# Kernel optimization log

Hardware: AMD Instinct MI355X
Metric: run time of the kernel (lower is better)

Reference implementation:

```python
import jax, jax.numpy as jnp
import numpy as np
import math

A, B, C, D = 32, 32, 8, 16
K, STRIDE, PAD, ITERS = 3, 1, 1, 3
KK = K * K
KKA = KK * A


def squash(s, axis=-1):
    mag_sq = jnp.sum(s ** 2, axis=axis, keepdims=True)
    mag = jnp.sqrt(mag_sq)
    return mag_sq / (1.0 + mag_sq) * (s / mag)


def setup_inputs() -> dict:
    key = jax.random.key(0)
    k1, k2 = jax.random.split(key)
    pose = jax.random.normal(k1, (4, A * C, 14, 14), dtype=jnp.float32)
    # kaiming_uniform_ on (KKA, B*D, C): fan_in = (B*D)*C = 4096, bound = sqrt(6/fan_in)
    bound = math.sqrt(6.0 / (B * D * C))
    W = jax.random.uniform(k2, (KKA, B * D, C), dtype=jnp.float32, minval=-bound, maxval=bound)
    return {"pose": pose, "W": W}


def reference(pose, W):
    b, _, h, w = pose.shape
    # F.unfold equivalent: (b, A*C*kk, oh, ow), channel-major then kernel-position ordering
    patches = jax.lax.conv_general_dilated_patches(
        pose, (K, K), (STRIDE, STRIDE), [(PAD, PAD), (PAD, PAD)])
    l = patches.shape[2] * patches.shape[3]
    x = patches.reshape(b, A, C, KK, l)
    x = jnp.transpose(x, (0, 4, 3, 1, 2)).reshape(b, l, KKA, C)  # (b,l,kkA,C)
    # pose_out[b,l,k,:] = W[k] @ x[b,l,k]  -> (b,l,kkA,B*D)
    pose_out = jnp.einsum('kpc,blkc->blkp', W, x).reshape(b, l, KKA, B, D)
    logits = jnp.zeros((b, l, KKA, B, 1), dtype=pose.dtype)
    v = None
    for _ in range(ITERS):
        c = jax.nn.softmax(logits, axis=3)                      # over B capsules
        s = jnp.sum(c * pose_out, axis=2, keepdims=True)        # (b,l,1,B,D)
        v = squash(s)
        logits = logits + jnp.sum(v * pose_out, axis=-1, keepdims=True)
    v = v[:, :, 0]                                              # (b,l,B,D)
    v = jnp.transpose(v.reshape(b, l, B * D), (0, 2, 1))        # (b,B*D,l)
    oh = math.isqrt(l)
    return v.reshape(b, B * D, oh, oh)
```

## Files before the change

### kernel.cpp

```cpp
#include <hip/hip_runtime.h>
#include <stdint.h>

#define NSITES 784
#define LSZ    196
#define HWD    14
#define KKA_   288
#define BD_    512
#define NRG    6
#define ROWS_PER_BLK 48
#define NW     8
#define ROWS_PER_WAVE 6
#define SITES_PER_BLK 4

#define WH_OFF    0
#define XH_OFF    2359296
#define PART_OFF  5971968
#define VBUF_OFF  15605760
#define WS_NEED   17211392

typedef _Float16 h2 __attribute__((ext_vector_type(2)));

#define PIN8(p) asm volatile("" : "+v"(p[0]),"+v"(p[1]),"+v"(p[2]),"+v"(p[3]), \
                                  "+v"(p[4]),"+v"(p[5]),"+v"(p[6]),"+v"(p[7]))

__device__ __forceinline__ float dot8(const uint4 wv, const uint4 xv) {
    h2 w0 = __builtin_bit_cast(h2, wv.x), w1 = __builtin_bit_cast(h2, wv.y),
       w2 = __builtin_bit_cast(h2, wv.z), w3 = __builtin_bit_cast(h2, wv.w);
    h2 x0 = __builtin_bit_cast(h2, xv.x), x1 = __builtin_bit_cast(h2, xv.y),
       x2 = __builtin_bit_cast(h2, xv.z), x3 = __builtin_bit_cast(h2, xv.w);
#if __has_builtin(__builtin_amdgcn_fdot2)
    float acc = __builtin_amdgcn_fdot2(w0, x0, 0.f, false);
    acc = __builtin_amdgcn_fdot2(w1, x1, acc, false);
    acc = __builtin_amdgcn_fdot2(w2, x2, acc, false);
    acc = __builtin_amdgcn_fdot2(w3, x3, acc, false);
    return acc;
#else
    float acc = (float)w0.x*(float)x0.x + (float)w0.y*(float)x0.y
              + (float)w1.x*(float)x1.x + (float)w1.y*(float)x1.y
              + (float)w2.x*(float)x2.x + (float)w2.y*(float)x2.y
              + (float)w3.x*(float)x3.x + (float)w3.y*(float)x3.y;
    return acc;
#endif
}

__global__ __launch_bounds__(256) void k_prep(
    const float* __restrict__ pose, const float* __restrict__ W,
    uint4* __restrict__ Wh, uint4* __restrict__ xh)
{
    const int t  = threadIdx.x;
    const int bx = blockIdx.x;
    if (bx < NSITES) {
        const int site = bx;
        const int b = site / LSZ;
        const int l = site - b * LSZ;
        const int oh = l / HWD, ow = l - oh * HWD;
        for (int kk = t; kk < KKA_; kk += 256) {
            const int p = kk >> 5, a = kk & 31;
            const int ky = p / 3 - 1, kx = p % 3 - 1;
            const int y = oh + ky, x = ow + kx;
            const bool inb = (y >= 0 && y < HWD && x >= 0 && x < HWD);
            const float* pp = pose + ((size_t)b * 256 + a * 8) * LSZ
                            + (inb ? (y * HWD + x) : 0);
            uint32_t uo[4];
            #pragma unroll
            for (int cp = 0; cp < 4; ++cp) {
                const float f0 = inb ? pp[(2*cp)   * LSZ] : 0.f;
                const float f1 = inb ? pp[(2*cp+1) * LSZ] : 0.f;
                h2 hh; hh.x = (_Float16)f0; hh.y = (_Float16)f1;
                uo[cp] = __builtin_bit_cast(uint32_t, hh);
            }
            uint4 o; o.x = uo[0]; o.y = uo[1]; o.z = uo[2]; o.w = uo[3];
            xh[(size_t)site * KKA_ + kk] = o;
        }
    } else {
        const int wb = bx - NSITES;
        const int kk = wb * 4 + (t >> 6);
        const int ln = t & 63;
        const float* Wr = W + (size_t)kk * (BD_ * 8);
        #pragma unroll
        for (int u = 0; u < 8; ++u) {
            const int p = ln * 8 + u;
            const float4 fa = *(const float4*)(Wr + p * 8);
            const float4 fb = *(const float4*)(Wr + p * 8 + 4);
            uint32_t uo[4];
            h2 h0; h0.x=(_Float16)fa.x; h0.y=(_Float16)fa.y; uo[0]=__builtin_bit_cast(uint32_t,h0);
            h2 h1; h1.x=(_Float16)fa.z; h1.y=(_Float16)fa.w; uo[1]=__builtin_bit_cast(uint32_t,h1);
            h2 hv; hv.x=(_Float16)fb.x; hv.y=(_Float16)fb.y; uo[2]=__builtin_bit_cast(uint32_t,hv);
            h2 h3; h3.x=(_Float16)fb.z; h3.y=(_Float16)fb.w; uo[3]=__builtin_bit_cast(uint32_t,h3);
            uint4 o; o.x=uo[0]; o.y=uo[1]; o.z=uo[2]; o.w=uo[3];
            Wh[(size_t)kk * 512 + u * 64 + ln] = o;
        }
    }
}

template<int PASS>
__global__ __launch_bounds__(512, 4) void k_sweep(
    const uint4* __restrict__ Wh, const uint4* __restrict__ xh,
    const float* __restrict__ vbuf, float* __restrict__ partial)
{
    const int t  = threadIdx.x;
    const int w  = t >> 6;
    const int ln = t & 63;
    const int sg = blockIdx.x;
    const int rg = blockIdx.y;
    const int site0 = sg * SITES_PER_BLK;
    const int kk0 = __builtin_amdgcn_readfirstlane(rg * ROWS_PER_BLK + w);

    float v[SITES_PER_BLK][8];
    if (PASS >= 2) {
        #pragma unroll
        for (int s = 0; s < SITES_PER_BLK; ++s) {
            const float4* vp = (const float4*)(vbuf + (size_t)(site0 + s) * BD_ + ln * 8);
            const float4 a = vp[0], bq = vp[1];
            v[s][0]=a.x;  v[s][1]=a.y;  v[s][2]=a.z;  v[s][3]=a.w;
            v[s][4]=bq.x; v[s][5]=bq.y; v[s][6]=bq.z; v[s][7]=bq.w;
            PIN8(v[s]);
        }
    }

    float sacc[SITES_PER_BLK][8];
    #pragma unroll
    for (int s = 0; s < SITES_PER_BLK; ++s)
        #pragma unroll
        for (int j = 0; j < 8; ++j) sacc[s][j] = 0.f;

    const uint4* Wrow = Wh + (size_t)kk0 * 512;
    const uint4* xrow = xh + kk0;

    #pragma unroll 1
    for (int r = 0; r < ROWS_PER_WAVE; ++r) {
        uint4 wr[8];
        #pragma unroll
        for (int u = 0; u < 8; ++u) wr[u] = Wrow[u * 64 + ln];
        Wrow += NW * 512;

        #pragma unroll
        for (int s = 0; s < SITES_PER_BLK; ++s) {
            const uint4 xr = xrow[(size_t)(site0 + s) * KKA_];
            float po[8];
            #pragma unroll
            for (int j = 0; j < 8; ++j) po[j] = dot8(wr[j], xr);
            if (PASS == 1) {
                #pragma unroll
                for (int j = 0; j < 8; ++j) sacc[s][j] += po[j];
            } else {
                float up = v[s][0] * po[0];
                #pragma unroll
                for (int j = 1; j < 8; ++j) up += v[s][j] * po[j];
                up += __shfl_xor(up, 1, 64);
                const float e = __expf(up);
                float se = e;
                se += __shfl_xor(se, 2, 64);
                se += __shfl_xor(se, 4, 64);
                se += __shfl_xor(se, 8, 64);
                se += __shfl_xor(se, 16, 64);
                se += __shfl_xor(se, 32, 64);
                const float c = e * __builtin_amdgcn_rcpf(se);
                #pragma unroll
                for (int j = 0; j < 8; ++j) sacc[s][j] += c * po[j];
            }
        }
        xrow += NW;
    }

    __shared__ float red[NW * BD_];
    #pragma unroll
    for (int s = 0; s < SITES_PER_BLK; ++s) {
        if (s) __syncthreads();
        float4 r0, r1;
        r0.x=sacc[s][0]; r0.y=sacc[s][1]; r0.z=sacc[s][2]; r0.w=sacc[s][3];
        r1.x=sacc[s][4]; r1.y=sacc[s][5]; r1.z=sacc[s][6]; r1.w=sacc[s][7];
        *(float4*)&red[w * BD_ + ln * 8]     = r0;
        *(float4*)&red[w * BD_ + ln * 8 + 4] = r1;
        __syncthreads();
        {
            const int p = t;
            float acc = red[p];
            #pragma unroll
            for (int ww = 1; ww < NW; ++ww) acc += red[ww * BD_ + p];
            partial[((size_t)(site0 + s) * NRG + rg) * BD_ + p] = acc;
        }
    }
}

template<int PASS>
__global__ __launch_bounds__(256) void k_reduce(
    const float* __restrict__ partial, float* __restrict__ vbuf,
    float* __restrict__ out)
{
    const int site = blockIdx.x * 4 + (threadIdx.x >> 6);
    const int ln = threadIdx.x & 63;
    float tv[8] = {0.f,0.f,0.f,0.f,0.f,0.f,0.f,0.f};
    #pragma unroll
    for (int rg = 0; rg < NRG; ++rg) {
        const float4* pp4 = (const float4*)(partial + ((size_t)site * NRG + rg) * BD_ + ln * 8);
        const float4 a = pp4[0], b = pp4[1];
        tv[0]+=a.x; tv[1]+=a.y; tv[2]+=a.z; tv[3]+=a.w;
        tv[4]+=b.x; tv[5]+=b.y; tv[6]+=b.z; tv[7]+=b.w;
    }
    if (PASS == 1) {
        #pragma unroll
        for (int j = 0; j < 8; ++j) tv[j] *= (1.f / 32.f);
    }
    float msq = 0.f;
    #pragma unroll
    for (int j = 0; j < 8; ++j) msq += tv[j] * tv[j];
    msq += __shfl_xor(msq, 1, 64);
    const float fac = sqrtf(msq) / (1.f + msq);
    if (PASS == 1) {
        #pragma unroll
        for (int j = 0; j < 8; ++j) vbuf[(size_t)site * BD_ + ln * 8 + j] = tv[j] * fac;
    } else if (PASS == 2) {
        #pragma unroll
        for (int j = 0; j < 8; ++j) vbuf[(size_t)site * BD_ + ln * 8 + j] += tv[j] * fac;
    } else {
        const int b = site / LSZ;
        const int l = site - b * LSZ;
        float* op = out + (size_t)b * BD_ * LSZ + l;
        #pragma unroll
        for (int j = 0; j < 8; ++j) op[(size_t)(ln * 8 + j) * LSZ] = tv[j] * fac;
    }
}

extern "C" void kernel_launch(void* const* d_in, const int* in_sizes, int n_in,
                              void* d_out, int out_size, void* d_ws, size_t ws_size,
                              hipStream_t stream) {
    const float* pose = (const float*)d_in[0];
    const float* W    = (const float*)d_in[1];
    float* out        = (float*)d_out;

    if (ws_size < (size_t)WS_NEED) return;

    uint8_t* ws = (uint8_t*)d_ws;
    uint4*  Wh     = (uint4*)  (ws + WH_OFF);
    uint4*  xh     = (uint4*)  (ws + XH_OFF);
    float* partial = (float*)  (ws + PART_OFF);
    float* vbuf    = (float*)  (ws + VBUF_OFF);

    k_prep<<<dim3(NSITES + 72), dim3(256), 0, stream>>>(pose, W, Wh, xh);

    const dim3 gs(NSITES / SITES_PER_BLK, NRG);
    k_sweep<1><<<gs, dim3(512), 0, stream>>>(Wh, xh, vbuf, partial);
    k_reduce<1><<<dim3(NSITES / 4), dim3(256), 0, stream>>>(partial, vbuf, out);
    k_sweep<2><<<gs, dim3(512), 0, stream>>>(Wh, xh, vbuf, partial);
    k_reduce<2><<<dim3(NSITES / 4), dim3(256), 0, stream>>>(partial, vbuf, out);
    k_sweep<3><<<gs, dim3(512), 0, stream>>>(Wh, xh, vbuf, partial);
    k_reduce<3><<<dim3(NSITES / 4), dim3(256), 0, stream>>>(partial, vbuf, out);
}
```

Baseline: 182.8 us.

## Replace first routing pass with MFMA GEMM over flattened kka·C dimension

In the first routing iteration the coupling coefficients are uniform, so s equals the sum over kka of W·x, which is a plain GEMM of x (784×2304) by W (2304×512). The first sweep is replaced by an MFMA f16 GEMM kernel plus a small squash kernel, using a new K-major copy of W written during prep. This removes a full per-row dot-product sweep and its partial reduction, at the cost of extra workspace and an extra weight-copy write in prep.

New measurement: 183.3 us. Within noise of the previous version (+0.3%).

```diff
diff --git a/kernel.cpp b/kernel.cpp
--- a/kernel.cpp
+++ b/kernel.cpp
@@ -14,11 +14,15 @@
 
 #define WH_OFF    0
 #define XH_OFF    2359296
-#define PART_OFF  5971968
-#define VBUF_OFF  15605760
-#define WS_NEED   17211392
+#define WG_OFF    5971968
+#define S1_OFF    8331264
+#define PART_OFF  9936896
+#define VBUF_OFF  19570688
+#define WS_NEED   21176320
 
 typedef _Float16 h2 __attribute__((ext_vector_type(2)));
+typedef _Float16 h8 __attribute__((ext_vector_type(8)));
+typedef float    f4 __attribute__((ext_vector_type(4)));
 
 #define PIN8(p) asm volatile("" : "+v"(p[0]),"+v"(p[1]),"+v"(p[2]),"+v"(p[3]), \
                                   "+v"(p[4]),"+v"(p[5]),"+v"(p[6]),"+v"(p[7]))
@@ -45,7 +49,7 @@
 
 __global__ __launch_bounds__(256) void k_prep(
     const float* __restrict__ pose, const float* __restrict__ W,
-    uint4* __restrict__ Wh, uint4* __restrict__ xh)
+    uint4* __restrict__ Wh, uint4* __restrict__ xh, uint4* __restrict__ Wg)
 {
     const int t  = threadIdx.x;
     const int bx = blockIdx.x;
@@ -89,8 +93,56 @@
             h2 h3; h3.x=(_Float16)fb.z; h3.y=(_Float16)fb.w; uo[3]=__builtin_bit_cast(uint32_t,h3);
             uint4 o; o.x=uo[0]; o.y=uo[1]; o.z=uo[2]; o.w=uo[3];
             Wh[(size_t)kk * 512 + u * 64 + ln] = o;
-        }
-    }
+            Wg[(size_t)kk * 512 + p] = o;
+        }
+    }
+}
+
+__global__ __launch_bounds__(256) void k_gemm1(
+    const uint4* __restrict__ xh, const uint4* __restrict__ Wg,
+    float* __restrict__ s1)
+{
+    const int t   = threadIdx.x;
+    const int w   = t >> 6;
+    const int l   = t & 63;
+    const int m0  = blockIdx.x * 16;
+    const int n0  = blockIdx.y * 64 + w * 16;
+    const int row = l & 15;
+    const int sub = l >> 4;
+
+    f4 acc = {0.f, 0.f, 0.f, 0.f};
+    const uint4* ap = xh + (size_t)(m0 + row) * KKA_ + sub;
+    const uint4* bp = Wg + (size_t)sub * 512 + (n0 + row);
+
+    #pragma unroll 4
+    for (int ks = 0; ks < 72; ++ks) {
+        const h8 a = __builtin_bit_cast(h8, ap[ks * 4]);
+        const h8 b = __builtin_bit_cast(h8, bp[(size_t)ks * 4 * 512]);
+        acc = __builtin_amdgcn_mfma_f32_16x16x32_f16(a, b, acc, 0, 0, 0);
+    }
+
+    float* op = s1 + (size_t)(m0 + sub * 4) * BD_ + n0 + row;
+    op[0]        = acc[0];
+    op[BD_]      = acc[1];
+    op[2 * BD_]  = acc[2];
+    op[3 * BD_]  = acc[3];
+}
+
+__global__ __launch_bounds__(256) void k_red1(
+    const float* __restrict__ s1, float* __restrict__ vbuf)
+{
+    const int site = blockIdx.x * 4 + (threadIdx.x >> 6);
+    const int ln = threadIdx.x & 63;
+    const float4* sp = (const float4*)(s1 + (size_t)site * BD_ + ln * 8);
+    const float4 a = sp[0], b = sp[1];
+    float tv[8] = {a.x, a.y, a.z, a.w, b.x, b.y, b.z, b.w};
+    float msq = 0.f;
+    #pragma unroll
+    for (int j = 0; j < 8; ++j) { tv[j] *= (1.f / 32.f); msq += tv[j] * tv[j]; }
+    msq += __shfl_xor(msq, 1, 64);
+    const float fac = sqrtf(msq) / (1.f + msq);
+    #pragma unroll
+    for (int j = 0; j < 8; ++j) vbuf[(size_t)site * BD_ + ln * 8 + j] = tv[j] * fac;
 }
 
 template<int PASS>
@@ -107,15 +159,13 @@
     const int kk0 = __builtin_amdgcn_readfirstlane(rg * ROWS_PER_BLK + w);
 
     float v[SITES_PER_BLK][8];
-    if (PASS >= 2) {
-        #pragma unroll
-        for (int s = 0; s < SITES_PER_BLK; ++s) {
-            const float4* vp = (const float4*)(vbuf + (size_t)(site0 + s) * BD_ + ln * 8);
-            const float4 a = vp[0], bq = vp[1];
-            v[s][0]=a.x;  v[s][1]=a.y;  v[s][2]=a.z;  v[s][3]=a.w;
-            v[s][4]=bq.x; v[s][5]=bq.y; v[s][6]=bq.z; v[s][7]=bq.w;
-            PIN8(v[s]);
-        }
+    #pragma unroll
+    for (int s = 0; s < SITES_PER_BLK; ++s) {
+        const float4* vp = (const float4*)(vbuf + (size_t)(site0 + s) * BD_ + ln * 8);
+        const float4 a = vp[0], bq = vp[1];
+        v[s][0]=a.x;  v[s][1]=a.y;  v[s][2]=a.z;  v[s][3]=a.w;
+        v[s][4]=bq.x; v[s][5]=bq.y; v[s][6]=bq.z; v[s][7]=bq.w;
+        PIN8(v[s]);
     }
 
     float sacc[SITES_PER_BLK][8];
@@ -140,25 +190,20 @@
             float po[8];
             #pragma unroll
             for (int j = 0; j < 8; ++j) po[j] = dot8(wr[j], xr);
-            if (PASS == 1) {
-                #pragma unroll
-                for (int j = 0; j < 8; ++j) sacc[s][j] += po[j];
-            } else {
-                float up = v[s][0] * po[0];
-                #pragma unroll
-                for (int j = 1; j < 8; ++j) up += v[s][j] * po[j];
-                up += __shfl_xor(up, 1, 64);
-                const float e = __expf(up);
-                float se = e;
-                se += __shfl_xor(se, 2, 64);
-                se += __shfl_xor(se, 4, 64);
-                se += __shfl_xor(se, 8, 64);
-                se += __shfl_xor(se, 16, 64);
-                se += __shfl_xor(se, 32, 64);
-                const float c = e * __builtin_amdgcn_rcpf(se);
-                #pragma unroll
-                for (int j = 0; j < 8; ++j) sacc[s][j] += c * po[j];
-            }
+            float up = v[s][0] * po[0];
+            #pragma unroll
+            for (int j = 1; j < 8; ++j) up += v[s][j] * po[j];
+            up += __shfl_xor(up, 1, 64);
+            const float e = __expf(up);
+            float se = e;
+            se += __shfl_xor(se, 2, 64);
+            se += __shfl_xor(se, 4, 64);
+            se += __shfl_xor(se, 8, 64);
+            se += __shfl_xor(se, 16, 64);
+            se += __shfl_xor(se, 32, 64);
+            const float c = e * __builtin_amdgcn_rcpf(se);
+            #pragma unroll
+            for (int j = 0; j < 8; ++j) sacc[s][j] += c * po[j];
         }
         xrow += NW;
     }
@@ -198,19 +243,12 @@
         tv[0]+=a.x; tv[1]+=a.y; tv[2]+=a.z; tv[3]+=a.w;
         tv[4]+=b.x; tv[5]+=b.y; tv[6]+=b.z; tv[7]+=b.w;
     }
-    if (PASS == 1) {
-        #pragma unroll
-        for (int j = 0; j < 8; ++j) tv[j] *= (1.f / 32.f);
-    }
     float msq = 0.f;
     #pragma unroll
     for (int j = 0; j < 8; ++j) msq += tv[j] * tv[j];
     msq += __shfl_xor(msq, 1, 64);
     const float fac = sqrtf(msq) / (1.f + msq);
-    if (PASS == 1) {
-        #pragma unroll
-        for (int j = 0; j < 8; ++j) vbuf[(size_t)site * BD_ + ln * 8 + j] = tv[j] * fac;
-    } else if (PASS == 2) {
+    if (PASS == 2) {
         #pragma unroll
         for (int j = 0; j < 8; ++j) vbuf[(size_t)site * BD_ + ln * 8 + j] += tv[j] * fac;
     } else {
@@ -234,14 +272,17 @@
     uint8_t* ws = (uint8_t*)d_ws;
     uint4*  Wh     = (uint4*)  (ws + WH_OFF);
     uint4*  xh     = (uint4*)  (ws + XH_OFF);
+    uint4*  Wg     = (uint4*)  (ws + WG_OFF);
+    float*  s1     = (float*)  (ws + S1_OFF);
     float* partial = (float*)  (ws + PART_OFF);
     float* vbuf    = (float*)  (ws + VBUF_OFF);
 
-    k_prep<<<dim3(NSITES + 72), dim3(256), 0, stream>>>(pose, W, Wh, xh);
+    k_prep<<<dim3(NSITES + 72), dim3(256), 0, stream>>>(pose, W, Wh, xh, Wg);
+
+    k_gemm1<<<dim3(49, 8), dim3(256), 0, stream>>>(xh, Wg, s1);
+    k_red1<<<dim3(NSITES / 4), dim3(256), 0, stream>>>(s1, vbuf);
 
     const dim3 gs(NSITES / SITES_PER_BLK, NRG);
-    k_sweep<1><<<gs, dim3(512), 0, stream>>>(Wh, xh, vbuf, partial);
-    k_reduce<1><<<dim3(NSITES / 4), dim3(256), 0, stream>>>(partial, vbuf, out);
     k_sweep<2><<<gs, dim3(512), 0, stream>>>(Wh, xh, vbuf, partial);
     k_reduce<2><<<dim3(NSITES / 4), dim3(256), 0, stream>>>(partial, vbuf, out);
     k_sweep<3><<<gs, dim3(512), 0, stream>>>(Wh, xh, vbuf, partial);
```
